# Optimization experiments

Hardware: AMD Instinct MI355X
Metric: run time of the kernel (lower is better)

## Reference

```python
import jax, jax.numpy as jnp
import numpy as np
import math

B, N, CS, CZ = 1, 512, 384, 128
GD = 16            # ipa_conf.c_hidden -> num 3D groups G
CH = GD * 3        # per-head hidden = 48
H = 8
PQ, PV = 8, 12
NF = 4             # num_frequencies
INF, EPS = 1e5, 1e-8
CZ4 = CZ // 4


def base_frequencies(num_freqs=NF, base=8.0, max_freq=1.0):
    fs = [min(base ** (-2 * i / num_freqs) * max_freq, max_freq) for i in range(num_freqs)]
    return jnp.asarray(fs, dtype=jnp.float32)


def hat(v):
    # v: [..., 3] -> skew-symmetric [..., 3, 3]
    x, y, z = v[..., 0], v[..., 1], v[..., 2]
    o = jnp.zeros_like(x)
    return jnp.stack([
        jnp.stack([o, -z, y], -1),
        jnp.stack([z, o, -x], -1),
        jnp.stack([-y, x, o], -1)], -2)


def setup_inputs() -> dict:
    key = jax.random.key(0)
    ks = jax.random.split(key, 24)
    std = 0.02
    hc = CH * H
    hpkv = H * (PQ + PV) * 3
    inp = {
        's': jax.random.normal(ks[0], (B, N, CS), jnp.float32),
        'z': jax.random.normal(ks[1], (B, N, N, CZ), jnp.float32),
        'rotvec': jax.random.normal(ks[2], (B, N, 3), jnp.float32),
        'mask': jnp.ones((B, N), jnp.float32),
        'wq': jax.random.normal(ks[3], (CS, hc), jnp.float32) * std,
        'bq': jnp.zeros((hc,), jnp.float32),
        'wkv': jax.random.normal(ks[4], (CS, 2 * hc), jnp.float32) * std,
        'bkv': jnp.zeros((2 * hc,), jnp.float32),
        'wkvp': jax.random.normal(ks[5], (CS, hpkv), jnp.float32) * std,
        'bkvp': jnp.zeros((hpkv,), jnp.float32),
        'wb': jax.random.normal(ks[6], (CZ, H), jnp.float32) * std,
        'bb': jnp.zeros((H,), jnp.float32),
        'wdz': jax.random.normal(ks[7], (CZ, CZ4), jnp.float32) * std,
        'bdz': jnp.zeros((CZ4,), jnp.float32),
        'wout': jax.random.normal(ks[8], (H * (CZ4 + CH + PV * 4), CS), jnp.float32) * std,
        'bout': jnp.zeros((CS,), jnp.float32),
        'log_freq_adj': jax.random.normal(ks[9], (NF,), jnp.float32) * std,
        'group_weights': jax.random.normal(ks[10], (GD,), jnp.float32) * std,
        'freq_weights': jnp.full((NF,), 1.0 / NF, jnp.float32),
    }
    return inp


def reference(s, z, rotvec, mask, wq, bq, wkv, bkv, wkvp, bkvp, wb, bb,
              wdz, bdz, wout, bout, log_freq_adj, group_weights, freq_weights):
    G = GD
    # projections
    q = (s @ wq + bq).reshape(B, N, H, CH)
    kv = (s @ wkv + bkv).reshape(B, N, H, 2 * CH)
    k, v = kv[..., :CH], kv[..., CH:]
    P = PQ + PV
    kvp = (s @ wkvp + bkvp).reshape(B, N, 3, H * P)      # torch split(...,3)+stack(-1)
    kvp = jnp.moveaxis(kvp, -2, -1).reshape(B, N, H, P, 3)
    v_pts = kvp[..., PQ:, :]                             # [B,N,H,PV,3]
    bias = z @ wb + bb                                   # [B,N,N,H]
    # RoPE-inspired multi-frequency Rodrigues rotations
    nrm = jnp.linalg.norm(rotvec, axis=-1, keepdims=True)
    angle = nrm + 1e-8                                   # [B,N,1]
    axis = rotvec / jnp.maximum(nrm, 1e-12)
    freqs = base_frequencies() * jnp.exp(log_freq_adj)   # [F]
    theta = angle * freqs                                # [B,N,F]
    K = hat(axis)                                        # [B,N,3,3]
    K2 = K @ K
    sin_t = jnp.sin(theta)[..., None, None]              # [B,N,F,1,1]
    cos_t = jnp.cos(theta)[..., None, None]
    I3 = jnp.eye(3, dtype=s.dtype)
    R = I3 + sin_t * K[:, :, None] + (1.0 - cos_t) * K2[:, :, None]  # [B,N,F,3,3]
    qg = q.reshape(B, N, H, G, 3)
    kg = k.reshape(B, N, H, G, 3)
    q_rot = jnp.einsum('bnfij,bnhgj->bnhgfi', R, qg)     # [B,N,H,G,F,3]
    k_rot = jnp.einsum('bnfij,bnhgj->bnhgfi', R, kg)
    # aggregation weights (sum over groups, softmax-weighted freqs)
    freq_w = jax.nn.softmax(freq_weights)
    group_w = jax.nn.softplus(group_weights) * math.sqrt(1.0 / G)
    qw = q_rot * freq_w[None, None, None, None, :, None] * group_w[None, None, None, :, None, None]
    scores = jnp.einsum('bihgfc,bjhgfc->bhij', qw, k_rot) / math.sqrt(3.0)
    a = scores + math.sqrt(1.0 / 3.0) * jnp.transpose(bias, (0, 3, 1, 2))
    sq_mask = INF * (mask[:, :, None] * mask[:, None, :] - 1.0)
    a = jax.nn.softmax(a + sq_mask[:, None], axis=-1)    # [B,H,N,N]
    # outputs
    o = jnp.einsum('bhij,bjhc->bihc', a, v).reshape(B, N, H * CH)
    o_pt = jnp.einsum('bhij,bjhpc->bihpc', a, v_pts)     # [B,N,H,PV,3]
    o_pt_norm = jnp.sqrt(jnp.sum(o_pt ** 2, -1) + EPS).reshape(B, N, H * PV)
    o_pt_flat = o_pt.reshape(B, N, H * PV, 3)
    pair_z = z @ wdz + bdz                               # [B,N,N,CZ4]
    o_pair = jnp.einsum('bhij,bijc->bihc', a, pair_z).reshape(B, N, H * CZ4)
    feats = jnp.concatenate([o, o_pt_flat[..., 0], o_pt_flat[..., 1],
                             o_pt_flat[..., 2], o_pt_norm, o_pair], axis=-1)
    return feats @ wout + bout                           # [B,N,CS]
```

## Files before the change

kernel.cpp:

```cpp
#include <hip/hip_runtime.h>
#include <math.h>


#define OFF_PROJ 0
#define SZ_PROJ (512*1632)
#define OFF_QW (OFF_PROJ + SZ_PROJ)
#define SZ_QW (8*512*192)
#define OFF_KST (OFF_QW + SZ_QW)
#define OFF_V (OFF_KST + SZ_QW)
#define SZ_V (512*384)
#define OFF_VP (OFF_V + SZ_V)
#define SZ_VP (512*288)
#define OFF_A (OFF_VP + SZ_VP)
#define SZ_A (8*512*512)
#define OFF_FEATS (OFF_A + SZ_A)
#define SZ_FEATS (512*1024)
#define OFF_PART (OFF_FEATS + SZ_FEATS)
#define SZ_PART (8*512*384)

__global__ __launch_bounds__(256) void proj_kernel(
    const float* __restrict__ s, const float* __restrict__ wq, const float* __restrict__ bq,
    const float* __restrict__ wkv, const float* __restrict__ bkv,
    const float* __restrict__ wkvp, const float* __restrict__ bkvp,
    float* __restrict__ proj)
{
  __shared__ float sT[384][34];
  int ct = blockIdx.x;
  int i0 = blockIdx.y * 32;
  int col0 = ct * 64;
  const float* W; const float* bias; int wld, wcol0;
  if (col0 < 384)       { W = wq;   bias = bq;   wld = 384; wcol0 = col0; }
  else if (col0 < 1152) { W = wkv;  bias = bkv;  wld = 768; wcol0 = col0 - 384; }
  else                  { W = wkvp; bias = bkvp; wld = 480; wcol0 = col0 - 1152; }
  int t = threadIdx.x;
  #pragma unroll
  for (int r = 0; r < 12; r++){
    int e = t + 256*r;
    int i = e & 31;
    int k4 = e >> 5;
    float4 v = *(const float4*)(s + (size_t)(i0 + i)*384 + k4*4);
    sT[k4*4+0][i] = v.x; sT[k4*4+1][i] = v.y; sT[k4*4+2][i] = v.z; sT[k4*4+3][i] = v.w;
  }
  __syncthreads();
  int cr = t & 15;
  int ipair = t >> 4;
  int ii = ipair * 2;
  int wc = wcol0 + cr*4;
  bool valid = (wc + 4 <= wld);
  int wcc = valid ? wc : (wld - 4);
  float acc[2][4];
  #pragma unroll
  for (int q = 0; q < 2; q++)
    #pragma unroll
    for (int p = 0; p < 4; p++) acc[q][p] = 0.f;
  #pragma unroll 4
  for (int k = 0; k < 384; k++){
    float2 a2 = *(const float2*)&sT[k][ii];
    float4 w4 = *(const float4*)(W + (size_t)k*wld + wcc);
    acc[0][0] = fmaf(a2.x, w4.x, acc[0][0]);
    acc[0][1] = fmaf(a2.x, w4.y, acc[0][1]);
    acc[0][2] = fmaf(a2.x, w4.z, acc[0][2]);
    acc[0][3] = fmaf(a2.x, w4.w, acc[0][3]);
    acc[1][0] = fmaf(a2.y, w4.x, acc[1][0]);
    acc[1][1] = fmaf(a2.y, w4.y, acc[1][1]);
    acc[1][2] = fmaf(a2.y, w4.z, acc[1][2]);
    acc[1][3] = fmaf(a2.y, w4.w, acc[1][3]);
  }
  if (valid){
    float4 bv = *(const float4*)(bias + wc);
    #pragma unroll
    for (int q = 0; q < 2; q++){
      int row = i0 + ii + q;
      float4 o;
      o.x = acc[q][0] + bv.x; o.y = acc[q][1] + bv.y;
      o.z = acc[q][2] + bv.z; o.w = acc[q][3] + bv.w;
      *(float4*)(proj + (size_t)row*1632 + col0 + cr*4) = o;
    }
  }
}

__global__ __launch_bounds__(128) void node_kernel(
    const float* __restrict__ proj, const float* __restrict__ rotvec,
    const float* __restrict__ lfa, const float* __restrict__ gwts, const float* __restrict__ fwts,
    float* __restrict__ Qw, float* __restrict__ Kst, float* __restrict__ V, float* __restrict__ VP)
{
  int i = blockIdx.x, t = threadIdx.x;
  const float* pr = proj + (size_t)i*1632;
  float rx = rotvec[i*3], ry = rotvec[i*3+1], rz = rotvec[i*3+2];
  float nrm = sqrtf(rx*rx + ry*ry + rz*rz);
  float angle = nrm + 1e-8f;
  float inv = 1.0f / fmaxf(nrm, 1e-12f);
  float ax = rx*inv, ay = ry*inv, az = rz*inv;
  float f0 = fwts[0], f1 = fwts[1], f2 = fwts[2], f3 = fwts[3];
  float mfw = fmaxf(fmaxf(f0,f1), fmaxf(f2,f3));
  float e0 = expf(f0-mfw), e1 = expf(f1-mfw), e2 = expf(f2-mfw), e3 = expf(f3-mfw);
  float esum = e0+e1+e2+e3;
  float fw[4] = {e0/esum, e1/esum, e2/esum, e3/esum};
  float fq[4] = { 1.0f*expf(lfa[0]), 0.35355339059327373f*expf(lfa[1]),
                  0.125f*expf(lfa[2]), 0.04419417382415922f*expf(lfa[3]) };
  int h = t >> 4, g = t & 15;
  float gw = log1pf(expf(gwts[g])) * 0.25f;
  float q0 = pr[h*48 + g*3 + 0], q1 = pr[h*48 + g*3 + 1], q2 = pr[h*48 + g*3 + 2];
  float k0 = pr[384 + h*96 + g*3 + 0], k1 = pr[384 + h*96 + g*3 + 1], k2 = pr[384 + h*96 + g*3 + 2];
  #pragma unroll
  for (int f = 0; f < 4; f++){
    float th = angle * fq[f];
    float sn = sinf(th), cs = cosf(th), omc = 1.0f - cs;
    float r00 = cs + omc*ax*ax,       r01 = omc*ax*ay - sn*az,  r02 = omc*ax*az + sn*ay;
    float r10 = omc*ay*ax + sn*az,    r11 = cs + omc*ay*ay,     r12 = omc*ay*az - sn*ax;
    float r20 = omc*az*ax - sn*ay,    r21 = omc*az*ay + sn*ax,  r22 = cs + omc*az*az;
    float qr0 = r00*q0 + r01*q1 + r02*q2;
    float qr1 = r10*q0 + r11*q1 + r12*q2;
    float qr2 = r20*q0 + r21*q1 + r22*q2;
    float kr0 = r00*k0 + r01*k1 + r02*k2;
    float kr1 = r10*k0 + r11*k1 + r12*k2;
    float kr2 = r20*k0 + r21*k1 + r22*k2;
    float sc = fw[f] * gw * 0.57735026918962576f;
    int base = (h*512 + i)*192 + (g*4 + f)*3;
    Qw[base+0] = qr0*sc; Qw[base+1] = qr1*sc; Qw[base+2] = qr2*sc;
    Kst[base+0] = kr0;   Kst[base+1] = kr1;   Kst[base+2] = kr2;
  }
  for (int c = t; c < 384; c += 128){
    int hh = c / 48, cc = c % 48;
    V[(size_t)i*384 + c] = pr[384 + hh*96 + 48 + cc];
  }
  for (int qx = t; qx < 288; qx += 128){
    int ch = qx / 3, c3 = qx % 3;
    int hh = ch / 12, p = ch % 12;
    VP[(size_t)i*288 + qx] = pr[1152 + c3*160 + hh*20 + 8 + p];
  }
}

__global__ __launch_bounds__(256) void zbias_kernel(
    const float* __restrict__ z, const float* __restrict__ wb, const float* __restrict__ bb,
    float* __restrict__ biasS)
{
  __shared__ float zs[8*1032];
  __shared__ float Wl[8*132];
  int i = blockIdx.y;
  int jt = blockIdx.x;
  int t = threadIdx.x;
  for (int r = 0; r < 4; r++){
    int e = t + 256*r;
    int ch = e & 7, k = e >> 3;
    Wl[ch*132 + k] = wb[k*8 + ch];
  }
  int cg = t >> 6, jg = t & 63;
  int ch0 = cg*2;
  float acc[2][4];
  #pragma unroll
  for (int c = 0; c < 2; c++)
    #pragma unroll
    for (int q = 0; q < 4; q++) acc[c][q] = 0.f;
  const float* zrow = z + ((size_t)i*512 + jt*256)*128;
  for (int kt = 0; kt < 4; kt++){
    __syncthreads();
    #pragma unroll
    for (int r = 0; r < 8; r++){
      int j = (t & 63) + 64*(r & 3);
      int kq = (t >> 6) + 4*(r >> 2);
      float4 v = *(const float4*)(zrow + (size_t)j*128 + kt*32 + kq*4);
      *(float4*)&zs[kq*1032 + j*4] = v;
    }
    __syncthreads();
    const float* wl0 = Wl + ch0*132 + kt*32;
    const float* wl1 = wl0 + 132;
    #pragma unroll
    for (int kq = 0; kq < 8; kq++){
      float4 w0 = *(const float4*)(wl0 + kq*4);
      float4 w1 = *(const float4*)(wl1 + kq*4);
      #pragma unroll
      for (int q = 0; q < 4; q++){
        float4 zv = *(const float4*)&zs[kq*1032 + (q*64 + jg)*4];
        acc[0][q] = fmaf(zv.x, w0.x, acc[0][q]);
        acc[0][q] = fmaf(zv.y, w0.y, acc[0][q]);
        acc[0][q] = fmaf(zv.z, w0.z, acc[0][q]);
        acc[0][q] = fmaf(zv.w, w0.w, acc[0][q]);
        acc[1][q] = fmaf(zv.x, w1.x, acc[1][q]);
        acc[1][q] = fmaf(zv.y, w1.y, acc[1][q]);
        acc[1][q] = fmaf(zv.z, w1.z, acc[1][q]);
        acc[1][q] = fmaf(zv.w, w1.w, acc[1][q]);
      }
    }
  }
  float b0 = bb[ch0], b1 = bb[ch0+1];
  #pragma unroll
  for (int q = 0; q < 4; q++){
    int j = jt*256 + q*64 + jg;
    biasS[(size_t)ch0*262144 + i*512 + j]     = 0.57735026918962576f * (acc[0][q] + b0);
    biasS[(size_t)(ch0+1)*262144 + i*512 + j] = 0.57735026918962576f * (acc[1][q] + b1);
  }
}

__global__ __launch_bounds__(256) void scores_kernel(
    const float* __restrict__ Qw, const float* __restrict__ Kst,
    const float* __restrict__ mask, float* A)
{
  __shared__ float Ks[4*2056];
  __shared__ float Qs[4*40];
  int i0 = blockIdx.x * 8;
  int h = blockIdx.y;
  int t = threadIdx.x;
  int ig = t >> 6, jl = t & 63;
  const float* Kb = Kst + (size_t)h*512*192;
  const float* Qb = Qw + (size_t)(h*512 + i0)*192;
  float acc[2][8];
  float mj[8];
  #pragma unroll
  for (int jt = 0; jt < 8; jt++) mj[jt] = mask[jt*64 + jl];
  #pragma unroll
  for (int q = 0; q < 2; q++){
    int i = i0 + ig*2 + q;
    float mi = mask[i];
    #pragma unroll
    for (int jt = 0; jt < 8; jt++){
      acc[q][jt] = A[((size_t)h*512 + i)*512 + jt*64 + jl] + 100000.0f*(mi*mj[jt] - 1.0f);
    }
  }
  for (int kc = 0; kc < 12; kc++){
    __syncthreads();
    {
      int k4 = t >> 6;
      #pragma unroll
      for (int r = 0; r < 8; r++){
        int j = (t & 63) + 64*r;
        float4 v = *(const float4*)(Kb + (size_t)j*192 + kc*16 + k4*4);
        *(float4*)&Ks[k4*2056 + j*4] = v;
      }
    }
    if (t < 32){
      int qi = t >> 2, k4 = t & 3;
      float4 v = *(const float4*)(Qb + (size_t)qi*192 + kc*16 + k4*4);
      *(float4*)&Qs[k4*40 + qi*4] = v;
    }
    __syncthreads();
    #pragma unroll
    for (int k4 = 0; k4 < 4; k4++){
      float4 qf[2];
      #pragma unroll
      for (int q = 0; q < 2; q++)
        qf[q] = *(const float4*)&Qs[k4*40 + (ig*2+q)*4];
      #pragma unroll
      for (int jt = 0; jt < 8; jt++){
        float4 kf = *(const float4*)&Ks[k4*2056 + (jt*64 + jl)*4];
        #pragma unroll
        for (int q = 0; q < 2; q++){
          acc[q][jt] = fmaf(qf[q].x, kf.x, acc[q][jt]);
          acc[q][jt] = fmaf(qf[q].y, kf.y, acc[q][jt]);
          acc[q][jt] = fmaf(qf[q].z, kf.z, acc[q][jt]);
          acc[q][jt] = fmaf(qf[q].w, kf.w, acc[q][jt]);
        }
      }
    }
  }
  #pragma unroll
  for (int q = 0; q < 2; q++){
    int i = i0 + ig*2 + q;
    float m = acc[q][0];
    #pragma unroll
    for (int jt = 1; jt < 8; jt++) m = fmaxf(m, acc[q][jt]);
    for (int off = 32; off > 0; off >>= 1) m = fmaxf(m, __shfl_xor(m, off));
    float ssum = 0.f;
    #pragma unroll
    for (int jt = 0; jt < 8; jt++){ acc[q][jt] = expf(acc[q][jt] - m); ssum += acc[q][jt]; }
    for (int off = 32; off > 0; off >>= 1) ssum += __shfl_xor(ssum, off);
    float invs = 1.0f / ssum;
    #pragma unroll
    for (int jt = 0; jt < 8; jt++){
      A[((size_t)h*512 + i)*512 + jt*64 + jl] = acc[q][jt] * invs;
    }
  }
}

__global__ __launch_bounds__(256) void attnout_kernel(
    const float* __restrict__ A, const float* __restrict__ z,
    const float* __restrict__ wdz, const float* __restrict__ bdz,
    const float* __restrict__ V, const float* __restrict__ VP,
    float* __restrict__ feats)
{
  __shared__ float a_s[2*512*10];
  __shared__ float Y_s[2*8*132];
  __shared__ float opt_s[2][292];
  int i0 = blockIdx.x * 2;
  int t = threadIdx.x;
  for (int r = 0; r < 32; r++){
    int e = t + 256*r;
    int hh = e >> 10, il = (e >> 9) & 1, j = e & 511;
    a_s[(il*512 + j)*10 + hh] = A[((size_t)hh*512 + i0 + il)*512 + j];
  }
  __syncthreads();
  {
    int il = t >> 7, u = t & 127, hg = u >> 5, k4 = u & 31;
    const float* zb = z + ((size_t)(i0 + il)*512)*128 + k4*4;
    const float* asb = a_s + il*5120 + hg*2;
    float acc0[4], acc1[4];
    #pragma unroll
    for (int m = 0; m < 4; m++){ acc0[m] = 0.f; acc1[m] = 0.f; }
    #pragma unroll 8
    for (int j = 0; j < 512; j++){
      float2 a2 = *(const float2*)&asb[j*10];
      float4 zv = *(const float4*)(zb + (size_t)j*128);
      acc0[0] = fmaf(a2.x, zv.x, acc0[0]);
      acc0[1] = fmaf(a2.x, zv.y, acc0[1]);
      acc0[2] = fmaf(a2.x, zv.z, acc0[2]);
      acc0[3] = fmaf(a2.x, zv.w, acc0[3]);
      acc1[0] = fmaf(a2.y, zv.x, acc1[0]);
      acc1[1] = fmaf(a2.y, zv.y, acc1[1]);
      acc1[2] = fmaf(a2.y, zv.z, acc1[2]);
      acc1[3] = fmaf(a2.y, zv.w, acc1[3]);
    }
    *(float4*)&Y_s[((il*8) + hg*2 + 0)*132 + k4*4] = make_float4(acc0[0],acc0[1],acc0[2],acc0[3]);
    *(float4*)&Y_s[((il*8) + hg*2 + 1)*132 + k4*4] = make_float4(acc1[0],acc1[1],acc1[2],acc1[3]);
  }
  __syncthreads();
  {
    int il = t >> 7, u = t & 127, hh = u >> 4, cp = u & 15;
    const float* Yr = Y_s + (il*8 + hh)*132;
    float s0 = bdz[cp*2], s1 = bdz[cp*2+1];
    #pragma unroll 8
    for (int k = 0; k < 128; k++){
      float yv = Yr[k];
      float2 w2 = *(const float2*)(wdz + (size_t)k*32 + cp*2);
      s0 = fmaf(yv, w2.x, s0);
      s1 = fmaf(yv, w2.y, s1);
    }
    float* fp = feats + (size_t)(i0 + il)*1024 + 768 + hh*32 + cp*2;
    fp[0] = s0; fp[1] = s1;
  }
  {
    bool act = (t < 168);
    const float* base = V; int stride = 384; int hh = 0;
    int ch = t*4;
    if (act){
      if (ch < 384){ hh = ch/48; base = V + ch; stride = 384; }
      else { int qq = ch - 384; hh = qq/36; base = VP + qq; stride = 288; }
    }
    float acc0[4], acc1[4];
    #pragma unroll
    for (int m = 0; m < 4; m++){ acc0[m] = 0.f; acc1[m] = 0.f; }
    if (act){
      const float* a0 = a_s + hh;
      const float* a1 = a_s + 5120 + hh;
      #pragma unroll 4
      for (int j = 0; j < 512; j++){
        float ax = a0[j*10];
        float ay = a1[j*10];
        float4 v4 = *(const float4*)(base + (size_t)j*stride);
        acc0[0] = fmaf(ax, v4.x, acc0[0]);
        acc0[1] = fmaf(ax, v4.y, acc0[1]);
        acc0[2] = fmaf(ax, v4.z, acc0[2]);
        acc0[3] = fmaf(ax, v4.w, acc0[3]);
        acc1[0] = fmaf(ay, v4.x, acc1[0]);
        acc1[1] = fmaf(ay, v4.y, acc1[1]);
        acc1[2] = fmaf(ay, v4.z, acc1[2]);
        acc1[3] = fmaf(ay, v4.w, acc1[3]);
      }
      if (ch < 384){
        *(float4*)&feats[(size_t)i0*1024 + ch]     = make_float4(acc0[0],acc0[1],acc0[2],acc0[3]);
        *(float4*)&feats[(size_t)(i0+1)*1024 + ch] = make_float4(acc1[0],acc1[1],acc1[2],acc1[3]);
      } else {
        int qq = ch - 384;
        #pragma unroll
        for (int m = 0; m < 4; m++){
          opt_s[0][qq + m] = acc0[m];
          opt_s[1][qq + m] = acc1[m];
        }
      }
    }
  }
  __syncthreads();
  if (t < 192){
    int il = t / 96, p = t % 96;
    float x = opt_s[il][p*3], y = opt_s[il][p*3+1], zz = opt_s[il][p*3+2];
    float* fr = feats + (size_t)(i0 + il)*1024;
    fr[384 + p] = x;
    fr[480 + p] = y;
    fr[576 + p] = zz;
    fr[672 + p] = sqrtf(x*x + y*y + zz*zz + 1e-8f);
  }
}

__global__ __launch_bounds__(256) void outgemm_kernel(
    const float* __restrict__ feats, const float* __restrict__ wout,
    float* __restrict__ part)
{
  __shared__ float fA[32*68];
  __shared__ float fB[32*68];
  int ct = blockIdx.x;
  int it = blockIdx.y;
  int sk = blockIdx.z;
  int i0 = it*64, c0 = ct*64, k0 = sk*128;
  int t = threadIdx.x;
  int ir = t >> 4, cr = t & 15;
  float acc[4][4];
  #pragma unroll
  for (int q = 0; q < 4; q++)
    #pragma unroll
    for (int p = 0; p < 4; p++) acc[q][p] = 0.f;
  for (int kt = 0; kt < 128; kt += 32){
    __syncthreads();
    #pragma unroll
    for (int r = 0; r < 2; r++){
      int e = t + 256*r;
      int i = e & 63, kq = e >> 6;
      float4 v = *(const float4*)(feats + (size_t)(i0 + i)*1024 + k0 + kt + kq*4);
      fA[(kq*4+0)*68 + i] = v.x; fA[(kq*4+1)*68 + i] = v.y;
      fA[(kq*4+2)*68 + i] = v.z; fA[(kq*4+3)*68 + i] = v.w;
    }
    #pragma unroll
    for (int r = 0; r < 2; r++){
      int e = t + 256*r;
      int kk = e >> 4, c4 = e & 15;
      float4 v = *(const float4*)(wout + (size_t)(k0 + kt + kk)*384 + c0 + c4*4);
      *(float4*)&fB[kk*68 + c4*4] = v;
    }
    __syncthreads();
    #pragma unroll 8
    for (int k = 0; k < 32; k++){
      float4 a4 = *(const float4*)&fA[k*68 + ir*4];
      float4 b4 = *(const float4*)&fB[k*68 + cr*4];
      acc[0][0] = fmaf(a4.x, b4.x, acc[0][0]);
      acc[0][1] = fmaf(a4.x, b4.y, acc[0][1]);
      acc[0][2] = fmaf(a4.x, b4.z, acc[0][2]);
      acc[0][3] = fmaf(a4.x, b4.w, acc[0][3]);
      acc[1][0] = fmaf(a4.y, b4.x, acc[1][0]);
      acc[1][1] = fmaf(a4.y, b4.y, acc[1][1]);
      acc[1][2] = fmaf(a4.y, b4.z, acc[1][2]);
      acc[1][3] = fmaf(a4.y, b4.w, acc[1][3]);
      acc[2][0] = fmaf(a4.z, b4.x, acc[2][0]);
      acc[2][1] = fmaf(a4.z, b4.y, acc[2][1]);
      acc[2][2] = fmaf(a4.z, b4.z, acc[2][2]);
      acc[2][3] = fmaf(a4.z, b4.w, acc[2][3]);
      acc[3][0] = fmaf(a4.w, b4.x, acc[3][0]);
      acc[3][1] = fmaf(a4.w, b4.y, acc[3][1]);
      acc[3][2] = fmaf(a4.w, b4.z, acc[3][2]);
      acc[3][3] = fmaf(a4.w, b4.w, acc[3][3]);
    }
  }
  float* pb = part + ((size_t)sk*512 + i0)*384 + c0;
  #pragma unroll
  for (int q = 0; q < 4; q++){
    float4 o;
    o.x = acc[q][0]; o.y = acc[q][1]; o.z = acc[q][2]; o.w = acc[q][3];
    *(float4*)&pb[(size_t)(ir*4 + q)*384 + cr*4] = o;
  }
}

__global__ __launch_bounds__(256) void outreduce_kernel(
    const float* __restrict__ part, const float* __restrict__ bout,
    float* __restrict__ out)
{
  int e = blockIdx.x*256 + threadIdx.x;
  float4 acc = *(const float4*)(bout + (e % 96)*4);
  #pragma unroll
  for (int sk = 0; sk < 8; sk++){
    float4 p = *(const float4*)(part + (size_t)sk*196608 + (size_t)e*4);
    acc.x += p.x; acc.y += p.y; acc.z += p.z; acc.w += p.w;
  }
  *(float4*)(out + (size_t)e*4) = acc;
}

extern "C" void kernel_launch(void* const* d_in, const int* in_sizes, int n_in,
                              void* d_out, int out_size, void* d_ws, size_t ws_size,
                              hipStream_t stream)
{
  const float* s    = (const float*)d_in[0];
  const float* z    = (const float*)d_in[1];
  const float* rotv = (const float*)d_in[2];
  const float* mask = (const float*)d_in[3];
  const float* wq   = (const float*)d_in[4];
  const float* bq   = (const float*)d_in[5];
  const float* wkv  = (const float*)d_in[6];
  const float* bkv  = (const float*)d_in[7];
  const float* wkvp = (const float*)d_in[8];
  const float* bkvp = (const float*)d_in[9];
  const float* wb   = (const float*)d_in[10];
  const float* bb   = (const float*)d_in[11];
  const float* wdz  = (const float*)d_in[12];
  const float* bdz  = (const float*)d_in[13];
  const float* wout = (const float*)d_in[14];
  const float* bout = (const float*)d_in[15];
  const float* lfa  = (const float*)d_in[16];
  const float* gwts = (const float*)d_in[17];
  const float* fwts = (const float*)d_in[18];
  float* out = (float*)d_out;
  float* ws  = (float*)d_ws;

  float* proj  = ws + OFF_PROJ;
  float* Qw    = ws + OFF_QW;
  float* Kst   = ws + OFF_KST;
  float* V     = ws + OFF_V;
  float* VP    = ws + OFF_VP;
  float* A     = ws + OFF_A;
  float* feats = ws + OFF_FEATS;
  float* part  = ws + OFF_PART;

  proj_kernel     <<<dim3(26, 16), 256, 0, stream>>>(s, wq, bq, wkv, bkv, wkvp, bkvp, proj);
  node_kernel     <<<dim3(512),    128, 0, stream>>>(proj, rotv, lfa, gwts, fwts, Qw, Kst, V, VP);
  zbias_kernel    <<<dim3(2, 512), 256, 0, stream>>>(z, wb, bb, A);
  scores_kernel   <<<dim3(64, 8),  256, 0, stream>>>(Qw, Kst, mask, A);
  attnout_kernel  <<<dim3(256),    256, 0, stream>>>(A, z, wdz, bdz, V, VP, feats);
  outgemm_kernel  <<<dim3(6, 8, 8),256, 0, stream>>>(feats, wout, part);
  outreduce_kernel<<<dim3(192),    256, 0, stream>>>(part, bout, out);
}
```

Before: 423.6 us.

## Split attention-output kernel into pair-z kernel and tiled per-head value GEMM

The fused attnout kernel is split in two. The pair part now runs one row per block (512 blocks) and splits the j range across two half-blocks, adding the partial sums in shared memory. The value and point-value outputs become a separate GEMM tiled through shared memory over 16 rows and one head, reading a concatenated per-head V/VP layout that node_kernel now writes. This reuses V across rows and spreads the work over more blocks than the old 2-row-per-block scheme, at the cost of an extra launch and reading A twice.

```diff
diff --git a/kernel.cpp b/kernel.cpp
--- a/kernel.cpp
+++ b/kernel.cpp
@@ -7,11 +7,9 @@
 #define OFF_QW (OFF_PROJ + SZ_PROJ)
 #define SZ_QW (8*512*192)
 #define OFF_KST (OFF_QW + SZ_QW)
-#define OFF_V (OFF_KST + SZ_QW)
-#define SZ_V (512*384)
-#define OFF_VP (OFF_V + SZ_V)
-#define SZ_VP (512*288)
-#define OFF_A (OFF_VP + SZ_VP)
+#define OFF_VCAT (OFF_KST + SZ_QW)
+#define SZ_VCAT (512*768)
+#define OFF_A (OFF_VCAT + SZ_VCAT)
 #define SZ_A (8*512*512)
 #define OFF_FEATS (OFF_A + SZ_A)
 #define SZ_FEATS (512*1024)
@@ -82,7 +80,7 @@
 __global__ __launch_bounds__(128) void node_kernel(
     const float* __restrict__ proj, const float* __restrict__ rotvec,
     const float* __restrict__ lfa, const float* __restrict__ gwts, const float* __restrict__ fwts,
-    float* __restrict__ Qw, float* __restrict__ Kst, float* __restrict__ V, float* __restrict__ VP)
+    float* __restrict__ Qw, float* __restrict__ Kst, float* __restrict__ Vcat)
 {
   int i = blockIdx.x, t = threadIdx.x;
   const float* pr = proj + (size_t)i*1632;
@@ -122,12 +120,12 @@
   }
   for (int c = t; c < 384; c += 128){
     int hh = c / 48, cc = c % 48;
-    V[(size_t)i*384 + c] = pr[384 + hh*96 + 48 + cc];
-  }
-  for (int qx = t; qx < 288; qx += 128){
-    int ch = qx / 3, c3 = qx % 3;
-    int hh = ch / 12, p = ch % 12;
-    VP[(size_t)i*288 + qx] = pr[1152 + c3*160 + hh*20 + 8 + p];
+    Vcat[(size_t)i*768 + hh*96 + cc] = pr[384 + hh*96 + 48 + cc];
+  }
+  for (int e = t; e < 288; e += 128){
+    int hh = e / 36, r = e % 36;
+    int p = r / 3, axv = r % 3;
+    Vcat[(size_t)i*768 + hh*96 + 48 + p*3 + axv] = pr[1152 + axv*160 + hh*20 + 8 + p];
   }
 }
 
@@ -272,111 +270,145 @@
   }
 }
 
-__global__ __launch_bounds__(256) void attnout_kernel(
+__global__ __launch_bounds__(256) void yopair_kernel(
     const float* __restrict__ A, const float* __restrict__ z,
     const float* __restrict__ wdz, const float* __restrict__ bdz,
-    const float* __restrict__ V, const float* __restrict__ VP,
     float* __restrict__ feats)
 {
-  __shared__ float a_s[2*512*10];
-  __shared__ float Y_s[2*8*132];
-  __shared__ float opt_s[2][292];
-  int i0 = blockIdx.x * 2;
+  __shared__ float a_s[512*10];
+  __shared__ float Y_s[8*132];
+  int i = blockIdx.x;
   int t = threadIdx.x;
-  for (int r = 0; r < 32; r++){
-    int e = t + 256*r;
-    int hh = e >> 10, il = (e >> 9) & 1, j = e & 511;
-    a_s[(il*512 + j)*10 + hh] = A[((size_t)hh*512 + i0 + il)*512 + j];
+  #pragma unroll
+  for (int r = 0; r < 4; r++){
+    int idx = t + r*256;
+    int h = idx >> 7, j4 = idx & 127;
+    float4 v = *(const float4*)(A + ((size_t)h*512 + i)*512 + j4*4);
+    a_s[(j4*4+0)*10 + h] = v.x;
+    a_s[(j4*4+1)*10 + h] = v.y;
+    a_s[(j4*4+2)*10 + h] = v.z;
+    a_s[(j4*4+3)*10 + h] = v.w;
   }
   __syncthreads();
-  {
-    int il = t >> 7, u = t & 127, hg = u >> 5, k4 = u & 31;
-    const float* zb = z + ((size_t)(i0 + il)*512)*128 + k4*4;
-    const float* asb = a_s + il*5120 + hg*2;
-    float acc0[4], acc1[4];
-    #pragma unroll
-    for (int m = 0; m < 4; m++){ acc0[m] = 0.f; acc1[m] = 0.f; }
-    #pragma unroll 8
-    for (int j = 0; j < 512; j++){
-      float2 a2 = *(const float2*)&asb[j*10];
-      float4 zv = *(const float4*)(zb + (size_t)j*128);
-      acc0[0] = fmaf(a2.x, zv.x, acc0[0]);
-      acc0[1] = fmaf(a2.x, zv.y, acc0[1]);
-      acc0[2] = fmaf(a2.x, zv.z, acc0[2]);
-      acc0[3] = fmaf(a2.x, zv.w, acc0[3]);
-      acc1[0] = fmaf(a2.y, zv.x, acc1[0]);
-      acc1[1] = fmaf(a2.y, zv.y, acc1[1]);
-      acc1[2] = fmaf(a2.y, zv.z, acc1[2]);
-      acc1[3] = fmaf(a2.y, zv.w, acc1[3]);
-    }
-    *(float4*)&Y_s[((il*8) + hg*2 + 0)*132 + k4*4] = make_float4(acc0[0],acc0[1],acc0[2],acc0[3]);
-    *(float4*)&Y_s[((il*8) + hg*2 + 1)*132 + k4*4] = make_float4(acc1[0],acc1[1],acc1[2],acc1[3]);
+  int jh = t >> 7;
+  int u = t & 127, hg = u >> 5, k4 = u & 31;
+  int h0 = hg*2;
+  const float* zb = z + ((size_t)i*512 + jh*256)*128 + k4*4;
+  const float* ap = a_s + (jh*256)*10 + h0;
+  float acc0[4], acc1[4];
+  #pragma unroll
+  for (int m = 0; m < 4; m++){ acc0[m] = 0.f; acc1[m] = 0.f; }
+  #pragma unroll 8
+  for (int j = 0; j < 256; j++){
+    float2 a2 = *(const float2*)&ap[j*10];
+    float4 zv = *(const float4*)(zb + (size_t)j*128);
+    acc0[0] = fmaf(a2.x, zv.x, acc0[0]);
+    acc0[1] = fmaf(a2.x, zv.y, acc0[1]);
+    acc0[2] = fmaf(a2.x, zv.z, acc0[2]);
+    acc0[3] = fmaf(a2.x, zv.w, acc0[3]);
+    acc1[0] = fmaf(a2.y, zv.x, acc1[0]);
+    acc1[1] = fmaf(a2.y, zv.y, acc1[1]);
+    acc1[2] = fmaf(a2.y, zv.z, acc1[2]);
+    acc1[3] = fmaf(a2.y, zv.w, acc1[3]);
+  }
+  if (jh == 0){
+    *(float4*)&Y_s[h0*132 + k4*4]     = make_float4(acc0[0],acc0[1],acc0[2],acc0[3]);
+    *(float4*)&Y_s[(h0+1)*132 + k4*4] = make_float4(acc1[0],acc1[1],acc1[2],acc1[3]);
   }
   __syncthreads();
-  {
-    int il = t >> 7, u = t & 127, hh = u >> 4, cp = u & 15;
-    const float* Yr = Y_s + (il*8 + hh)*132;
-    float s0 = bdz[cp*2], s1 = bdz[cp*2+1];
-    #pragma unroll 8
-    for (int k = 0; k < 128; k++){
-      float yv = Yr[k];
-      float2 w2 = *(const float2*)(wdz + (size_t)k*32 + cp*2);
-      s0 = fmaf(yv, w2.x, s0);
-      s1 = fmaf(yv, w2.y, s1);
-    }
-    float* fp = feats + (size_t)(i0 + il)*1024 + 768 + hh*32 + cp*2;
-    fp[0] = s0; fp[1] = s1;
-  }
-  {
-    bool act = (t < 168);
-    const float* base = V; int stride = 384; int hh = 0;
-    int ch = t*4;
-    if (act){
-      if (ch < 384){ hh = ch/48; base = V + ch; stride = 384; }
-      else { int qq = ch - 384; hh = qq/36; base = VP + qq; stride = 288; }
-    }
-    float acc0[4], acc1[4];
-    #pragma unroll
-    for (int m = 0; m < 4; m++){ acc0[m] = 0.f; acc1[m] = 0.f; }
-    if (act){
-      const float* a0 = a_s + hh;
-      const float* a1 = a_s + 5120 + hh;
-      #pragma unroll 4
-      for (int j = 0; j < 512; j++){
-        float ax = a0[j*10];
-        float ay = a1[j*10];
-        float4 v4 = *(const float4*)(base + (size_t)j*stride);
-        acc0[0] = fmaf(ax, v4.x, acc0[0]);
-        acc0[1] = fmaf(ax, v4.y, acc0[1]);
-        acc0[2] = fmaf(ax, v4.z, acc0[2]);
-        acc0[3] = fmaf(ax, v4.w, acc0[3]);
-        acc1[0] = fmaf(ay, v4.x, acc1[0]);
-        acc1[1] = fmaf(ay, v4.y, acc1[1]);
-        acc1[2] = fmaf(ay, v4.z, acc1[2]);
-        acc1[3] = fmaf(ay, v4.w, acc1[3]);
-      }
-      if (ch < 384){
-        *(float4*)&feats[(size_t)i0*1024 + ch]     = make_float4(acc0[0],acc0[1],acc0[2],acc0[3]);
-        *(float4*)&feats[(size_t)(i0+1)*1024 + ch] = make_float4(acc1[0],acc1[1],acc1[2],acc1[3]);
-      } else {
-        int qq = ch - 384;
-        #pragma unroll
-        for (int m = 0; m < 4; m++){
-          opt_s[0][qq + m] = acc0[m];
-          opt_s[1][qq + m] = acc1[m];
-        }
+  if (jh == 1){
+    float4 p0 = *(const float4*)&Y_s[h0*132 + k4*4];
+    float4 p1 = *(const float4*)&Y_s[(h0+1)*132 + k4*4];
+    p0.x += acc0[0]; p0.y += acc0[1]; p0.z += acc0[2]; p0.w += acc0[3];
+    p1.x += acc1[0]; p1.y += acc1[1]; p1.z += acc1[2]; p1.w += acc1[3];
+    *(float4*)&Y_s[h0*132 + k4*4]     = p0;
+    *(float4*)&Y_s[(h0+1)*132 + k4*4] = p1;
+  }
+  __syncthreads();
+  int h = t >> 5, c = t & 31;
+  float sacc = bdz[c];
+  const float* Yr = Y_s + h*132;
+  #pragma unroll 8
+  for (int k = 0; k < 128; k++){
+    sacc = fmaf(Yr[k], wdz[(size_t)k*32 + c], sacc);
+  }
+  feats[(size_t)i*1024 + 768 + h*32 + c] = sacc;
+}
+
+__global__ __launch_bounds__(256) void ovgemm_kernel(
+    const float* __restrict__ A, const float* __restrict__ Vcat,
+    float* __restrict__ feats)
+{
+  __shared__ float A_s[64*18];
+  __shared__ float V_s[64*100];
+  __shared__ float opt[16*40];
+  int i0 = blockIdx.x * 16;
+  int h = blockIdx.y;
+  int t = threadIdx.x;
+  int ip = t >> 5;
+  int cg = t & 31;
+  float acc[2][4];
+  #pragma unroll
+  for (int q = 0; q < 2; q++)
+    #pragma unroll
+    for (int m = 0; m < 4; m++) acc[q][m] = 0.f;
+  for (int cb = 0; cb < 512; cb += 64){
+    __syncthreads();
+    {
+      int ii = t >> 4, j4 = t & 15;
+      float4 v = *(const float4*)(A + ((size_t)h*512 + i0 + ii)*512 + cb + j4*4);
+      A_s[(j4*4+0)*18 + ii] = v.x;
+      A_s[(j4*4+1)*18 + ii] = v.y;
+      A_s[(j4*4+2)*18 + ii] = v.z;
+      A_s[(j4*4+3)*18 + ii] = v.w;
+    }
+    #pragma unroll
+    for (int r = 0; r < 6; r++){
+      int idx = t + r*256;
+      int j = idx / 24, cq = idx % 24;
+      float4 v = *(const float4*)(Vcat + (size_t)(cb + j)*768 + h*96 + cq*4);
+      *(float4*)&V_s[j*100 + cq*4] = v;
+    }
+    __syncthreads();
+    #pragma unroll 4
+    for (int k = 0; k < 64; k++){
+      float2 a2 = *(const float2*)&A_s[k*18 + ip*2];
+      float4 v4 = *(const float4*)&V_s[k*100 + cg*4];
+      acc[0][0] = fmaf(a2.x, v4.x, acc[0][0]);
+      acc[0][1] = fmaf(a2.x, v4.y, acc[0][1]);
+      acc[0][2] = fmaf(a2.x, v4.z, acc[0][2]);
+      acc[0][3] = fmaf(a2.x, v4.w, acc[0][3]);
+      acc[1][0] = fmaf(a2.y, v4.x, acc[1][0]);
+      acc[1][1] = fmaf(a2.y, v4.y, acc[1][1]);
+      acc[1][2] = fmaf(a2.y, v4.z, acc[1][2]);
+      acc[1][3] = fmaf(a2.y, v4.w, acc[1][3]);
+    }
+  }
+  int c0 = cg*4;
+  if (c0 < 48){
+    #pragma unroll
+    for (int q = 0; q < 2; q++){
+      *(float4*)&feats[(size_t)(i0 + ip*2 + q)*1024 + h*48 + c0] =
+        make_float4(acc[q][0], acc[q][1], acc[q][2], acc[q][3]);
+    }
+  } else if (c0 < 84){
+    #pragma unroll
+    for (int q = 0; q < 2; q++){
+      #pragma unroll
+      for (int m = 0; m < 4; m++){
+        opt[(ip*2+q)*40 + (c0 - 48 + m)] = acc[q][m];
       }
     }
   }
   __syncthreads();
   if (t < 192){
-    int il = t / 96, p = t % 96;
-    float x = opt_s[il][p*3], y = opt_s[il][p*3+1], zz = opt_s[il][p*3+2];
+    int il = t / 12, p = t % 12;
+    float x = opt[il*40 + p*3], y = opt[il*40 + p*3 + 1], zz = opt[il*40 + p*3 + 2];
     float* fr = feats + (size_t)(i0 + il)*1024;
-    fr[384 + p] = x;
-    fr[480 + p] = y;
-    fr[576 + p] = zz;
-    fr[672 + p] = sqrtf(x*x + y*y + zz*zz + 1e-8f);
+    fr[384 + h*12 + p] = x;
+    fr[480 + h*12 + p] = y;
+    fr[576 + h*12 + p] = zz;
+    fr[672 + h*12 + p] = sqrtf(x*x + y*y + zz*zz + 1e-8f);
   }
 }
 
@@ -489,17 +521,17 @@
   float* proj  = ws + OFF_PROJ;
   float* Qw    = ws + OFF_QW;
   float* Kst   = ws + OFF_KST;
-  float* V     = ws + OFF_V;
-  float* VP    = ws + OFF_VP;
+  float* Vcat  = ws + OFF_VCAT;
   float* A     = ws + OFF_A;
   float* feats = ws + OFF_FEATS;
   float* part  = ws + OFF_PART;
 
   proj_kernel     <<<dim3(26, 16), 256, 0, stream>>>(s, wq, bq, wkv, bkv, wkvp, bkvp, proj);
-  node_kernel     <<<dim3(512),    128, 0, stream>>>(proj, rotv, lfa, gwts, fwts, Qw, Kst, V, VP);
+  node_kernel     <<<dim3(512),    128, 0, stream>>>(proj, rotv, lfa, gwts, fwts, Qw, Kst, Vcat);
   zbias_kernel    <<<dim3(2, 512), 256, 0, stream>>>(z, wb, bb, A);
   scores_kernel   <<<dim3(64, 8),  256, 0, stream>>>(Qw, Kst, mask, A);
-  attnout_kernel  <<<dim3(256),    256, 0, stream>>>(A, z, wdz, bdz, V, VP, feats);
+  yopair_kernel   <<<dim3(512),    256, 0, stream>>>(A, z, wdz, bdz, feats);
+  ovgemm_kernel   <<<dim3(32, 8),  256, 0, stream>>>(A, Vcat, feats);
   outgemm_kernel  <<<dim3(6, 8, 8),256, 0, stream>>>(feats, wout, part);
   outreduce_kernel<<<dim3(192),    256, 0, stream>>>(part, bout, out);
 }
```

Result: faster. 391.5 us (-7.6%).
